# Kernel optimization log

Hardware: AMD Instinct MI355X
Metric: run time of the kernel (lower is better)

The kernel has to match this reference:

```python
import jax, jax.numpy as jnp
import numpy as np

CIN, HID, OUT = 128, 256, 349
NTYPES, ETYPES = 4, 5
N0, N1, N2 = 120000, 40000, 10000
GNODES, GEDGES = 250000, 2000000
E0, E1 = 1500000, 400000


def setup_inputs() -> dict:
    key = jax.random.key(0)
    ks = jax.random.split(key, 24)
    ri = jax.random.randint
    rn = jax.random.normal
    inp = {}
    inp['n_id'] = ri(ks[0], (N0,), 0, GNODES)
    inp['x0'] = rn(ks[1], (100000, CIN), dtype=jnp.float32)
    inp['src0'] = ri(ks[2], (E0,), 0, N0)
    inp['dst0'] = ri(ks[3], (E0,), 0, N1)
    inp['e_id0'] = ri(ks[4], (E0,), 0, GEDGES)
    inp['src1'] = ri(ks[5], (E1,), 0, N1)
    inp['dst1'] = ri(ks[6], (E1,), 0, N2)
    inp['e_id1'] = ri(ks[7], (E1,), 0, GEDGES)
    inp['edge_type'] = ri(ks[8], (GEDGES,), 0, ETYPES)
    inp['node_type'] = ri(ks[9], (GNODES,), 0, NTYPES)
    inp['local_node_idx'] = ri(ks[10], (GNODES,), 0, 50000)
    # learned parameters
    inp['emb1'] = rn(ks[11], (50000, CIN), dtype=jnp.float32)
    inp['emb2'] = rn(ks[12], (50000, CIN), dtype=jnp.float32)
    inp['emb3'] = rn(ks[13], (50000, CIN), dtype=jnp.float32)
    s0 = 1.0 / np.sqrt(CIN)
    s1 = 1.0 / np.sqrt(HID)
    inp['relW0'] = rn(ks[14], (ETYPES, CIN, HID), dtype=jnp.float32) * s0
    inp['rootW0'] = rn(ks[15], (NTYPES, CIN, HID), dtype=jnp.float32) * s0
    inp['rootb0'] = rn(ks[16], (NTYPES, HID), dtype=jnp.float32) * 0.02
    inp['relW1'] = rn(ks[17], (ETYPES, HID, OUT), dtype=jnp.float32) * s1
    inp['rootW1'] = rn(ks[18], (NTYPES, HID, OUT), dtype=jnp.float32) * s1
    inp['rootb1'] = rn(ks[19], (NTYPES, OUT), dtype=jnp.float32) * 0.02
    return inp


def _group_input(tables, node_type, local_node_idx, n_id):
    # RGNN.group_input: per-node-type gather from feature / embedding tables.
    nt = node_type[n_id]            # [N0]
    li = local_node_idx[n_id]       # [N0]
    h = jnp.zeros((n_id.shape[0], CIN), dtype=tables[0].dtype)
    for k, tab in enumerate(tables):
        idx = jnp.minimum(li, tab.shape[0] - 1)
        h = jnp.where((nt == k)[:, None], tab[idx], h)
    return h, nt


def _rgcn_layer(x, nt_src, src, dst, et, relW, rootW, rootb, n_tgt):
    # out = sum_t mean-aggregate(x_j over edges of type t) @ W_t  (linear commutes with mean)
    T = relW.shape[0]
    xj = x[src]                                           # [E, Cin] gather
    seg = dst * T + et                                    # fused (target, edge_type) segment id
    sums = jax.ops.segment_sum(xj, seg, num_segments=n_tgt * T)
    cnts = jax.ops.segment_sum(jnp.ones((src.shape[0],), x.dtype), seg, num_segments=n_tgt * T)
    mean = (sums / jnp.maximum(cnts, 1.0)[:, None]).reshape(n_tgt, T, -1)  # [Nt, T, Cin]
    out = jnp.einsum('ntc,tco->no', mean, relW)           # [Nt, Cout]
    # per-node-type root linear: out[mask] += root_lins[i](x_target[mask])
    x_t = x[:n_tgt]
    nt_t = nt_src[:n_tgt]
    allr = jnp.einsum('nc,tco->tno', x_t, rootW) + rootb[:, None, :]  # [Tn, Nt, Cout]
    root = jnp.take_along_axis(allr, nt_t[None, :, None], axis=0)[0]
    return out + root


def reference(n_id, x0, src0, dst0, e_id0, src1, dst1, e_id1, edge_type, node_type,
              local_node_idx, emb1, emb2, emb3, relW0, rootW0, rootb0, relW1, rootW1, rootb1):
    h, nt = _group_input([x0, emb1, emb2, emb3], node_type, local_node_idx, n_id)
    # layer 0: I -> H
    h = _rgcn_layer(h, nt, src0, dst0, edge_type[e_id0], relW0, rootW0, rootb0, N1)
    h = jax.nn.relu(h)
    nt = nt[:N1]
    # layer 1: H -> O
    h = _rgcn_layer(h, nt, src1, dst1, edge_type[e_id1], relW1, rootW1, rootb1, N2)
    return jax.nn.log_softmax(h, axis=-1)
```

## Files before the change

kernel.cpp:

```cpp
#include <hip/hip_runtime.h>
#include <hip/hip_bf16.h>
#include <cmath>

constexpr int kCIN = 128, kHID = 256, kOUT = 349;
constexpr int kNT = 4, kET = 5;
constexpr int kN0 = 120000, kN1 = 40000, kN2 = 10000;
constexpr int kNSEG0 = kN1 * kET;
constexpr int kNSEG1 = kN2 * kET;
constexpr int kNSEG = kNSEG0 + kNSEG1;

constexpr int kBinSegs = 512;
constexpr int kNBin0 = (kNSEG0 + kBinSegs - 1) / kBinSegs;
constexpr int kNBin1 = (kNSEG1 + kBinSegs - 1) / kBinSegs;
constexpr int kNBin  = kNBin0 + kNBin1;
constexpr int kNBLK  = 512;
constexpr int kSB    = 128;
constexpr int kGB    = (kN0 + 31) / 32;

typedef __bf16 bf16x8 __attribute__((ext_vector_type(8)));
typedef float f32x4 __attribute__((ext_vector_type(4)));
typedef float f32x2v __attribute__((ext_vector_type(2)));
typedef unsigned short ushort8v __attribute__((ext_vector_type(8)));

__device__ __forceinline__ unsigned short f2b(float f) {
    unsigned int b = __float_as_uint(f);
    unsigned int r = (b + 0x7FFFu + ((b >> 16) & 1u)) >> 16;
    return (unsigned short)r;
}
__device__ __forceinline__ float b2f(unsigned short u) {
    return __uint_as_float((unsigned int)u << 16);
}
__device__ __forceinline__ void gl2lds16(const void* g, void* l) {
    __builtin_amdgcn_global_load_lds(
        (const __attribute__((address_space(1))) void*)g,
        (__attribute__((address_space(3))) void*)l, 16, 0, 0);
}

__device__ __forceinline__ unsigned int f2e4m3(float f) {
#if __has_builtin(__builtin_amdgcn_cvt_pk_fp8_f32)
    return (unsigned int)(__builtin_amdgcn_cvt_pk_fp8_f32(f, f, 0, false) & 0xFF);
#else
    unsigned int sb = (__float_as_uint(f) >> 31) << 7;
    float m = fminf(fabsf(f), 448.f);
    unsigned int code;
    if (m < 0.015625f) {
        code = (unsigned int)__float2int_rn(m * 512.f);
    } else {
        unsigned int b = __float_as_uint(m);
        b = b + 0x7FFFF + ((b >> 20) & 1);
        int e8 = (int)(b >> 23) - 120;
        if (e8 > 15) code = 0x7E;
        else code = ((unsigned int)e8 << 3) | ((b >> 20) & 7);
    }
    return sb | code;
#endif
}

__device__ __forceinline__ void e4m3x4_to_f32(unsigned int u, float* o4) {
#if __has_builtin(__builtin_amdgcn_cvt_pk_f32_fp8)
    f32x2v a = __builtin_amdgcn_cvt_pk_f32_fp8(u, false);
    f32x2v b = __builtin_amdgcn_cvt_pk_f32_fp8(u, true);
    o4[0] = a[0]; o4[1] = a[1]; o4[2] = b[0]; o4[3] = b[1];
#else
#pragma unroll
    for (int i = 0; i < 4; i++) {
        unsigned int c = (u >> (8 * i)) & 0xFF;
        unsigned int s = c >> 7, e = (c >> 3) & 15, mm = c & 7;
        float v;
        if (e == 0) v = (float)mm * 0.001953125f;
        else        v = __uint_as_float((e + 120u) << 23 | mm << 20);
        o4[i] = s ? -v : v;
    }
#endif
}

__global__ void k_prep(const float* __restrict__ relW0, const float* __restrict__ rootW0,
                       unsigned short* __restrict__ Bt0T,
                       const float* __restrict__ relW1, const float* __restrict__ rootW1,
                       unsigned short* __restrict__ Bt1T,
                       const int* __restrict__ etype, unsigned char* __restrict__ et8, int nET)
{
    constexpr int T0 = kNT * 256 * 768;
    constexpr int T1 = kNT * 384 * 1536;
    constexpr int TP = T0 + T1;
    int i = blockIdx.x * 256 + threadIdx.x;
    if (i < T0) {
        int g = i / (256 * 768);
        int rem = i - g * (256 * 768);
        int col = rem / 768;
        int k = rem - col * 768;
        float v = (k < 640) ? relW0[(size_t)k * 256 + col]
                            : rootW0[((size_t)g * 128 + (k - 640)) * 256 + col];
        Bt0T[i] = f2b(v);
    } else if (i < TP) {
        int ii = i - T0;
        int g = ii / (384 * 1536);
        int rem = ii - g * (384 * 1536);
        int col = rem / 1536;
        int k = rem - col * 1536;
        float v = 0.f;
        if (col < kOUT) v = (k < 1280) ? relW1[(size_t)k * kOUT + col]
                                       : rootW1[((size_t)g * 256 + (k - 1280)) * kOUT + col];
        Bt1T[ii] = f2b(v);
    } else {
        int k = i - TP;
        if (k < nET) et8[k] = (unsigned char)etype[k];
    }
}

__global__ __launch_bounds__(1024) void k_bincnt(
    const int* __restrict__ dst0, const int* __restrict__ eid0, int E0,
    const int* __restrict__ dst1, const int* __restrict__ eid1, int E1,
    const unsigned char* __restrict__ et8, int* __restrict__ cnts2d,
    int* __restrict__ seg32,
    const int* __restrict__ n_id, const int* __restrict__ ntype, int* __restrict__ ntcnts,
    const float* __restrict__ x0, const float* __restrict__ e1f,
    const float* __restrict__ e2f, const float* __restrict__ e3f,
    const int* __restrict__ lidx,
    unsigned short* __restrict__ h0b, unsigned char* __restrict__ h0f8,
    int* __restrict__ nt0)
{
    __shared__ int h[kNBin];
    const int tid = threadIdx.x;
    if (blockIdx.x < kNBLK) {
        for (int k = tid; k < kNBin; k += 1024) h[k] = 0;
        __syncthreads();
        int Etot = E0 + E1;
        int chunk = (Etot + kNBLK - 1) / kNBLK;
        int lo = blockIdx.x * chunk;
        int hi = min(lo + chunk, Etot);
        for (int i = lo + tid; i < hi; i += 1024) {
            int c;
            if (i < E0) c = dst0[i] * kET + (int)et8[eid0[i]];
            else { int e = i - E0; c = kNBin0 * kBinSegs + dst1[e] * kET + (int)et8[eid1[e]]; }
            seg32[i] = c;
            atomicAdd(&h[c >> 9], 1);
        }
        __syncthreads();
        for (int k = tid; k < kNBin; k += 1024) cnts2d[(size_t)k * kNBLK + blockIdx.x] = h[k];
    } else if (blockIdx.x < kNBLK + 2 * kSB) {
        int b = blockIdx.x - kNBLK;
        int layer = b >= kSB;
        int blk = b - layer * kSB;
        int M = layer ? kN2 : kN1;
        if (tid < 4) h[tid] = 0;
        __syncthreads();
        int chunk = (M + kSB - 1) / kSB;
        int lo = blk * chunk, hi = min(lo + chunk, M);
        for (int i = lo + tid; i < hi; i += 1024) atomicAdd(&h[ntype[n_id[i]]], 1);
        __syncthreads();
        if (tid < 4) ntcnts[(layer * 4 + tid) * kSB + blk] = h[tid];
    } else {
        int row = (blockIdx.x - kNBLK - 2 * kSB) * 32 + (tid >> 5);
        if (row >= kN0) return;
        int lane = tid & 31;
        int gid = n_id[row];
        int nt = ntype[gid];
        int li = lidx[gid];
        const float* tab;
        int rows;
        if (nt == 0)      { tab = x0;  rows = 100000; }
        else if (nt == 1) { tab = e1f; rows = 50000; }
        else if (nt == 2) { tab = e2f; rows = 50000; }
        else              { tab = e3f; rows = 50000; }
        int idx = li < rows ? li : rows - 1;
        float4 v = reinterpret_cast<const float4*>(tab + (size_t)idx * kCIN)[lane];
        ushort4 o;
        o.x = f2b(v.x); o.y = f2b(v.y); o.z = f2b(v.z); o.w = f2b(v.w);
        reinterpret_cast<ushort4*>(h0b + (size_t)row * kCIN)[lane] = o;
        unsigned int q = f2e4m3(v.x) | (f2e4m3(v.y) << 8) | (f2e4m3(v.z) << 16) | (f2e4m3(v.w) << 24);
        reinterpret_cast<unsigned int*>(h0f8 + (size_t)row * kCIN)[lane] = q;
        if (lane == 0) nt0[row] = nt;
    }
}

__global__ void k_scan1(const int* __restrict__ cnt, int* __restrict__ excl,
                        int* __restrict__ blksum, int n)
{
    __shared__ int sm[1024];
    int i = blockIdx.x * 1024 + threadIdx.x;
    int v = (i < n) ? cnt[i] : 0;
    sm[threadIdx.x] = v;
    __syncthreads();
    for (int off = 1; off < 1024; off <<= 1) {
        int t = (threadIdx.x >= off) ? sm[threadIdx.x - off] : 0;
        __syncthreads();
        sm[threadIdx.x] += t;
        __syncthreads();
    }
    if (i < n) excl[i] = sm[threadIdx.x] - v;
    if (threadIdx.x == 1023) blksum[blockIdx.x] = sm[1023];
}

__global__ __launch_bounds__(1024) void k_scan2(
    int* __restrict__ blksum, int nblk,
    const int* __restrict__ ntcnts, int* __restrict__ ntoffs,
    int* __restrict__ goff0, int* __restrict__ goff1)
{
    __shared__ int sm[1024];
    int tid = threadIdx.x;
    if (blockIdx.x == 0) {
        int v = (tid < nblk) ? blksum[tid] : 0;
        sm[tid] = v;
        __syncthreads();
        for (int off = 1; off < 1024; off <<= 1) {
            int t = (tid >= off) ? sm[tid - off] : 0;
            __syncthreads();
            sm[tid] += t;
            __syncthreads();
        }
        if (tid < nblk) blksum[tid] = sm[tid] - v;
    } else {
        int v = ntcnts[tid];
        sm[tid] = v;
        __syncthreads();
        for (int off = 1; off < 512; off <<= 1) {
            int t = 0;
            if ((tid & 511) >= off) t = sm[tid - off];
            __syncthreads();
            sm[tid] += t;
            __syncthreads();
        }
        int excl = sm[tid] - v;
        ntoffs[tid] = excl;
        if ((tid & 127) == 0) {
            int layer = tid >> 9;
            int t = (tid >> 7) & 3;
            if (layer == 0) goff0[t] = excl; else goff1[t] = excl;
        }
        if (tid == 0) { goff0[4] = kN1; goff1[4] = kN2; }
    }
}

__global__ __launch_bounds__(1024) void k_binplace(
    const int* __restrict__ src0, int E0,
    const int* __restrict__ src1, int E1,
    const int* __restrict__ seg32,
    const int* __restrict__ offs2d, const int* __restrict__ blksum,
    unsigned int* __restrict__ pairs,
    const int* __restrict__ nt0, const int* __restrict__ ntoffs,
    int* __restrict__ perm0, int* __restrict__ perm1)
{
    __shared__ int cur[kNBin];
    const int tid = threadIdx.x;
    if (blockIdx.x < kNBLK) {
        for (int k = tid; k < kNBin; k += 1024) {
            size_t li = (size_t)k * kNBLK + blockIdx.x;
            cur[k] = offs2d[li] + blksum[li >> 10];
        }
        __syncthreads();
        int Etot = E0 + E1;
        int chunk = (Etot + kNBLK - 1) / kNBLK;
        int lo = blockIdx.x * chunk;
        int hi = min(lo + chunk, Etot);
        for (int i = lo + tid; i < hi; i += 1024) {
            int c = seg32[i];
            int s = (i < E0) ? src0[i] : src1[i - E0];
            unsigned int pay = (unsigned int)s | ((unsigned int)(c & (kBinSegs - 1)) << 17);
            int p = atomicAdd(&cur[c >> 9], 1);
            pairs[p] = pay;
        }
    } else {
        int b = blockIdx.x - kNBLK;
        int layer = b >= kSB;
        int blk = b - layer * kSB;
        int M = layer ? kN2 : kN1;
        int* perm = layer ? perm1 : perm0;
        if (tid < 4) cur[tid] = ntoffs[(layer * 4 + tid) * kSB + blk];
        __syncthreads();
        int chunk = (M + kSB - 1) / kSB;
        int lo = blk * chunk, hi = min(lo + chunk, M);
        for (int i = lo + tid; i < hi; i += 1024) {
            int p = atomicAdd(&cur[nt0[i]], 1);
            perm[p] = i;
        }
    }
}

__global__ __launch_bounds__(1024) void k_binscatter(
    const int* __restrict__ offs2d, const int* __restrict__ blksum, int Etot,
    const unsigned int* __restrict__ pairs,
    int* __restrict__ order, int* __restrict__ starts, int* __restrict__ cnt)
{
    __shared__ int h[kBinSegs];
    __shared__ int sc[kBinSegs];
    __shared__ int cur[kBinSegs];
    const int bin = blockIdx.x;
    const int tid = threadIdx.x;
    size_t bi = (size_t)bin * kNBLK;
    const int base = offs2d[bi] + blksum[bi >> 10];
    int end = Etot;
    if (bin + 1 < kNBin) {
        size_t ei = (size_t)(bin + 1) * kNBLK;
        end = offs2d[ei] + blksum[ei >> 10];
    }
    const int c = end - base;
    const unsigned int* pp = pairs + base;

    for (int k = tid; k < kBinSegs; k += 1024) h[k] = 0;
    __syncthreads();
    for (int j = tid; j < c; j += 1024) atomicAdd(&h[pp[j] >> 17], 1);
    __syncthreads();
    if (tid < kBinSegs) sc[tid] = h[tid];
    __syncthreads();
    for (int off = 1; off < kBinSegs; off <<= 1) {
        int t = 0;
        if (tid < kBinSegs && tid >= off) t = sc[tid - off];
        __syncthreads();
        if (tid < kBinSegs) sc[tid] += t;
        __syncthreads();
    }
    int seg_rel, abs_base, seglim;
    if (bin < kNBin0) { seg_rel = bin * kBinSegs; abs_base = seg_rel; seglim = kNSEG0 - seg_rel; }
    else { seg_rel = (bin - kNBin0) * kBinSegs; abs_base = kNSEG0 + seg_rel; seglim = kNSEG1 - seg_rel; }
    if (tid < kBinSegs) {
        int excl = sc[tid] - h[tid];
        cur[tid] = excl;
        if (tid < seglim) {
            starts[abs_base + tid] = base + excl;
            cnt[abs_base + tid] = h[tid];
        }
    }
    __syncthreads();
    for (int j = tid; j < c; j += 1024) {
        unsigned int u = pp[j];
        int sl = (int)(u >> 17);
        int p = atomicAdd(&cur[sl], 1);
        order[base + p] = (int)(u & 0x1FFFFu);
    }
}

template<int C>
__global__ __launch_bounds__(256) void k_segreduce8(
    const int* __restrict__ starts, const int* __restrict__ cnt,
    const int* __restrict__ order, const unsigned char* __restrict__ h8,
    unsigned short* __restrict__ mean, int nseg)
{
    constexpr int L = C / 16;
    constexpr int SPB = 256 / L;
    int sidx = blockIdx.x * SPB + threadIdx.x / L;
    if (sidx >= nseg) return;
    int lane = threadIdx.x % L;
    int st = starts[sidx];
    int n = cnt[sidx];
    const unsigned char* hp = h8 + (size_t)lane * 16;
    float a0[16], a1[16];
#pragma unroll
    for (int i = 0; i < 16; i++) { a0[i] = 0.f; a1[i] = 0.f; }
    int j = 0;
    for (; j + 2 <= n; j += 2) {
        int s0 = order[st + j + 0];
        int s1 = order[st + j + 1];
        uint4 u0 = *reinterpret_cast<const uint4*>(hp + (size_t)s0 * C);
        uint4 u1 = *reinterpret_cast<const uint4*>(hp + (size_t)s1 * C);
        float d[16];
        e4m3x4_to_f32(u0.x, d); e4m3x4_to_f32(u0.y, d + 4);
        e4m3x4_to_f32(u0.z, d + 8); e4m3x4_to_f32(u0.w, d + 12);
#pragma unroll
        for (int i = 0; i < 16; i++) a0[i] += d[i];
        e4m3x4_to_f32(u1.x, d); e4m3x4_to_f32(u1.y, d + 4);
        e4m3x4_to_f32(u1.z, d + 8); e4m3x4_to_f32(u1.w, d + 12);
#pragma unroll
        for (int i = 0; i < 16; i++) a1[i] += d[i];
    }
    if (j < n) {
        int s0 = order[st + j];
        uint4 u0 = *reinterpret_cast<const uint4*>(hp + (size_t)s0 * C);
        float d[16];
        e4m3x4_to_f32(u0.x, d); e4m3x4_to_f32(u0.y, d + 4);
        e4m3x4_to_f32(u0.z, d + 8); e4m3x4_to_f32(u0.w, d + 12);
#pragma unroll
        for (int i = 0; i < 16; i++) a0[i] += d[i];
    }
    float sc = 1.0f / fmaxf((float)n, 1.0f);
    ushort8v o0, o1;
#pragma unroll
    for (int i = 0; i < 8; i++) {
        o0[i] = f2b((a0[i] + a1[i]) * sc);
        o1[i] = f2b((a0[i + 8] + a1[i + 8]) * sc);
    }
    unsigned short* mp = mean + (size_t)sidx * C + lane * 16;
    *reinterpret_cast<ushort8v*>(mp) = o0;
    *reinterpret_cast<ushort8v*>(mp + 8) = o1;
}

template<int C, int BM, int BNF, int NCB, int WR, int WC, int RELU, int OUTBF16, int OUTF8>
__global__ __launch_bounds__(256) void k_gemm_sorted(
    int M, int Nreal, int NpadK,
    const unsigned short* __restrict__ meanb,
    const unsigned short* __restrict__ hb,
    const unsigned short* __restrict__ BtT,
    const float* __restrict__ rootb,
    const int* __restrict__ perm, const int* __restrict__ goff,
    unsigned short* __restrict__ outb, float* __restrict__ outf,
    unsigned char* __restrict__ outf8)
{
    constexpr int K1 = kET * C;
    constexpr int K  = K1 + C;
    constexpr int FM = BM / (16 * WR);
    constexpr int FN = BNF / (16 * WC);
    __shared__ __align__(16) char ldsA[BM * 128];
    __shared__ __align__(16) char ldsB[BNF * 128];

    int nwg = gridDim.x;
    int orig = blockIdx.x;
    int q = nwg >> 3, r8 = nwg & 7, x8 = orig & 7;
    int logical = (x8 < r8 ? x8 * (q + 1) : r8 * (q + 1) + (x8 - r8) * q) + (orig >> 3);
    int colb = logical % NCB;
    int t = logical / NCB;

    int g, row0s = 0, gend = 0;
    {
        int gs[5] = {goff[0], goff[1], goff[2], goff[3], goff[4]};
        int tb = 0;
        for (g = 0; g < 4; ++g) {
            int cg = gs[g + 1] - gs[g];
            int ntl = (cg + BM - 1) / BM;
            if (t < tb + ntl) { row0s = gs[g] + (t - tb) * BM; gend = gs[g + 1]; break; }
            tb += ntl;
        }
        if (g == 4) return;
    }
    const int rows_here = min(BM, gend - row0s);
    const unsigned short* BtG = BtT + (size_t)g * NpadK;

    const int tid = threadIdx.x;
    const int col0 = colb * BNF;
    const int wid = tid >> 6, lane = tid & 63;
    const int wrow = (wid / WC) * (BM / WR);
    const int wcol = (wid % WC) * (BNF / WC);
    const int lr = lane >> 3;
    const int kb = (lane & 7) * 16;

    f32x4 acc[FM][FN] = {};

    for (int k0 = 0; k0 < K; k0 += 64) {
        const bool inMean = (k0 < K1);
        const size_t kB = (size_t)k0 * 2;
#pragma unroll
        for (int c2 = 0; c2 < BM / 32; ++c2) {
            int rb = (wid * (BM / 32) + c2) * 8;
            int r = rb + lr;
            int pr = perm[row0s + min(r, rows_here - 1)];
            const char* rowp = inMean
                ? (const char*)(meanb + (size_t)pr * K1) + kB
                : (const char*)(hb + (size_t)pr * C) + (kB - (size_t)K1 * 2);
            gl2lds16(rowp + (kb ^ ((r & 7) << 4)), &ldsA[rb * 128]);
        }
#pragma unroll
        for (int c2 = 0; c2 < BNF / 32; ++c2) {
            int rb = (wid * (BNF / 32) + c2) * 8;
            int r = rb + lr;
            const char* rowp = (const char*)(BtG + (size_t)(col0 + r) * K) + kB;
            gl2lds16(rowp + (kb ^ ((r & 7) << 4)), &ldsB[rb * 128]);
        }
        __syncthreads();
#pragma unroll
        for (int kc = 0; kc < 2; kc++) {
            int kb2 = kc * 64 + (lane >> 4) * 16;
            bf16x8 af[FM], bfr[FN];
#pragma unroll
            for (int m = 0; m < FM; m++) {
                int r = wrow + m * 16 + (lane & 15);
                af[m] = *reinterpret_cast<const bf16x8*>(&ldsA[r * 128 + (kb2 ^ ((r & 7) << 4))]);
            }
#pragma unroll
            for (int n = 0; n < FN; n++) {
                int r = wcol + n * 16 + (lane & 15);
                bfr[n] = *reinterpret_cast<const bf16x8*>(&ldsB[r * 128 + (kb2 ^ ((r & 7) << 4))]);
            }
#pragma unroll
            for (int m = 0; m < FM; m++)
#pragma unroll
                for (int n = 0; n < FN; n++)
                    acc[m][n] = __builtin_amdgcn_mfma_f32_16x16x32_bf16(af[m], bfr[n], acc[m][n], 0, 0, 0);
        }
        __syncthreads();
    }

#pragma unroll
    for (int m = 0; m < FM; m++) {
        int rlb = wrow + m * 16 + (lane >> 4) * 4;
#pragma unroll
        for (int n = 0; n < FN; n++) {
            int col = col0 + wcol + n * 16 + (lane & 15);
            if (col >= Nreal) continue;
            f32x4 v = acc[m][n];
#pragma unroll
            for (int j = 0; j < 4; j++) {
                int rl = rlb + j;
                if (rl >= rows_here) continue;
                int orig_row = perm[row0s + rl];
                float xv = v[j] + rootb[g * Nreal + col];
                if (RELU) xv = fmaxf(xv, 0.f);
                if (OUTBF16) {
                    outb[(size_t)orig_row * Nreal + col] = f2b(xv);
                    if (OUTF8) outf8[(size_t)orig_row * Nreal + col] = (unsigned char)f2e4m3(xv);
                } else {
                    outf[(size_t)orig_row * Nreal + col] = xv;
                }
            }
        }
    }
}

__global__ void k_logsm(float* __restrict__ out, int M, int N)
{
    int row = blockIdx.x * 4 + (threadIdx.x >> 6);
    if (row >= M) return;
    int lane = threadIdx.x & 63;
    float* p = out + (size_t)row * N;
    float mx = -3.4e38f;
    for (int c = lane; c < N; c += 64) mx = fmaxf(mx, p[c]);
#pragma unroll
    for (int o = 32; o > 0; o >>= 1) mx = fmaxf(mx, __shfl_xor(mx, o));
    float s = 0.f;
    for (int c = lane; c < N; c += 64) s += expf(p[c] - mx);
#pragma unroll
    for (int o = 32; o > 0; o >>= 1) s += __shfl_xor(s, o);
    float lse = mx + logf(s);
    for (int c = lane; c < N; c += 64) p[c] -= lse;
}

extern "C" void kernel_launch(void* const* d_in, const int* in_sizes, int n_in,
                              void* d_out, int out_size, void* d_ws, size_t ws_size,
                              hipStream_t stream)
{
    const int*   n_id   = (const int*)d_in[0];
    const float* x0     = (const float*)d_in[1];
    const int*   src0   = (const int*)d_in[2];
    const int*   dst0   = (const int*)d_in[3];
    const int*   eid0   = (const int*)d_in[4];
    const int*   src1   = (const int*)d_in[5];
    const int*   dst1   = (const int*)d_in[6];
    const int*   eid1   = (const int*)d_in[7];
    const int*   etype  = (const int*)d_in[8];
    const int*   ntype  = (const int*)d_in[9];
    const int*   lidx   = (const int*)d_in[10];
    const float* emb1   = (const float*)d_in[11];
    const float* emb2   = (const float*)d_in[12];
    const float* emb3   = (const float*)d_in[13];
    const float* relW0  = (const float*)d_in[14];
    const float* rootW0 = (const float*)d_in[15];
    const float* rootb0 = (const float*)d_in[16];
    const float* relW1  = (const float*)d_in[17];
    const float* rootW1 = (const float*)d_in[18];
    const float* rootb1 = (const float*)d_in[19];
    float* out = (float*)d_out;

    const int E0 = in_sizes[2];
    const int E1 = in_sizes[5];
    const int Etot = E0 + E1;
    const int nET = in_sizes[8];
    constexpr int K0s  = kET * kCIN + kCIN;
    constexpr int K1s  = kET * kHID + kHID;
    constexpr int Npad0 = 256;
    constexpr int Npad1 = 384;

    char* ws = (char*)d_ws;
    size_t off = 0;
    auto alloc = [&](size_t bytes) -> void* {
        void* p = ws + off;
        off = (off + bytes + 255) & ~(size_t)255;
        return p;
    };
    unsigned short* h0b   = (unsigned short*)alloc((size_t)kN0 * kCIN * 2);
    unsigned char*  h0f8  = (unsigned char*)alloc((size_t)kN0 * kCIN);
    int*            nt0   = (int*)alloc((size_t)kN0 * 4);
    unsigned short* meanb = (unsigned short*)alloc((size_t)kNSEG0 * kCIN * 2);
    int*            cnt    = (int*)alloc((size_t)kNSEG * 4);
    int*            starts = (int*)alloc((size_t)kNSEG * 4);
    int*            cnts2d = (int*)alloc((size_t)kNBin * kNBLK * 4);
    int*            offs2d = (int*)alloc((size_t)kNBin * kNBLK * 4);
    int*            blksum = (int*)alloc(1024 * 4);
    unsigned int*   pairs  = (unsigned int*)alloc((size_t)Etot * 4);
    int*            order  = (int*)alloc((size_t)Etot * 4);
    int*            seg32  = (int*)alloc((size_t)Etot * 4);
    unsigned char*  et8    = (unsigned char*)alloc((size_t)nET);
    unsigned short* h1b   = (unsigned short*)alloc((size_t)kN1 * kHID * 2);
    unsigned char*  h1f8  = (unsigned char*)alloc((size_t)kN1 * kHID);
    unsigned short* Bt0T  = (unsigned short*)alloc((size_t)kNT * Npad0 * K0s * 2);
    unsigned short* Bt1T  = (unsigned short*)alloc((size_t)kNT * Npad1 * K1s * 2);
    int*            perm0  = (int*)alloc((size_t)kN1 * 4);
    int*            goff0  = (int*)alloc(8 * 4);
    int*            perm1  = (int*)alloc((size_t)kN2 * 4);
    int*            goff1  = (int*)alloc(8 * 4);
    int*            ntcnts = (int*)alloc(1024 * 4);
    int*            ntoffs = (int*)alloc(1024 * 4);

    constexpr int TPREP = kNT * Npad0 * K0s + kNT * Npad1 * K1s;
    int prep_total = TPREP + nET;
    k_prep<<<(prep_total + 255) / 256, 256, 0, stream>>>(relW0, rootW0, Bt0T, relW1, rootW1, Bt1T,
                                                         etype, et8, nET);

    k_bincnt<<<kNBLK + 2 * kSB + kGB, 1024, 0, stream>>>(
        dst0, eid0, E0, dst1, eid1, E1, et8, cnts2d, seg32,
        n_id, ntype, ntcnts, x0, emb1, emb2, emb3, lidx, h0b, h0f8, nt0);

    int nscan = kNBin * kNBLK;
    int nblk = (nscan + 1023) / 1024;
    k_scan1<<<nblk, 1024, 0, stream>>>(cnts2d, offs2d, blksum, nscan);
    k_scan2<<<2, 1024, 0, stream>>>(blksum, nblk, ntcnts, ntoffs, goff0, goff1);
    k_binplace<<<kNBLK + 2 * kSB, 1024, 0, stream>>>(src0, E0, src1, E1, seg32,
                                                     offs2d, blksum, pairs, nt0, ntoffs, perm0, perm1);
    k_binscatter<<<kNBin, 1024, 0, stream>>>(offs2d, blksum, Etot, pairs, order, starts, cnt);

    k_segreduce8<kCIN><<<(kNSEG0 + 31) / 32, 256, 0, stream>>>(starts, cnt, order, h0f8, meanb, kNSEG0);
    int g0 = (kN1 / 64 + 4) * 2;
    k_gemm_sorted<kCIN, 64, 128, 2, 2, 2, 1, 1, 1><<<g0, 256, 0, stream>>>(
        kN1, kHID, Npad0 * K0s, meanb, h0b, Bt0T, rootb0, perm0, goff0, h1b, nullptr, h1f8);

    k_segreduce8<kHID><<<(kNSEG1 + 15) / 16, 256, 0, stream>>>(starts + kNSEG0, cnt + kNSEG0, order, h1f8, meanb, kNSEG1);
    int g1 = (kN2 / 64 + 5) * 3;
    k_gemm_sorted<kHID, 64, 128, 3, 2, 2, 0, 0, 0><<<g1, 256, 0, stream>>>(
        kN2, kOUT, Npad1 * K1s, meanb, h1b, Bt1T, rootb1, perm1, goff1, nullptr, out, nullptr);

    k_logsm<<<(kN2 + 3) / 4, 256, 0, stream>>>(out, kN2, kOUT);
}
```

Measured before the change: 236.3 us.

## Drop bf16 hidden copy, feed layer-1 root GEMM from fp8; two rows per gather warp

Layer 0 now writes only the fp8 hidden activations, dropping the separate bf16 copy. Layer 1's root-term A tiles are decoded from fp8 to bf16 in registers and stored to LDS, replacing the async global-to-LDS load. The input gather now handles two rows per half-warp to raise memory-level parallelism, and the binning block count is halved. This removes about 20 MB of writes but lowers root-term precision to fp8 and adds decode work inside the GEMM K-loop.

```diff
diff --git a/kernel.cpp b/kernel.cpp
--- a/kernel.cpp
+++ b/kernel.cpp
@@ -13,9 +13,9 @@
 constexpr int kNBin0 = (kNSEG0 + kBinSegs - 1) / kBinSegs;
 constexpr int kNBin1 = (kNSEG1 + kBinSegs - 1) / kBinSegs;
 constexpr int kNBin  = kNBin0 + kNBin1;
-constexpr int kNBLK  = 512;
+constexpr int kNBLK  = 256;
 constexpr int kSB    = 128;
-constexpr int kGB    = (kN0 + 31) / 32;
+constexpr int kGB    = kN0 / 64;
 
 typedef __bf16 bf16x8 __attribute__((ext_vector_type(8)));
 typedef float f32x4 __attribute__((ext_vector_type(4)));
@@ -151,26 +151,37 @@
         __syncthreads();
         if (tid < 4) ntcnts[(layer * 4 + tid) * kSB + blk] = h[tid];
     } else {
-        int row = (blockIdx.x - kNBLK - 2 * kSB) * 32 + (tid >> 5);
-        if (row >= kN0) return;
+        int base = (blockIdx.x - kNBLK - 2 * kSB) * 64;
         int lane = tid & 31;
-        int gid = n_id[row];
-        int nt = ntype[gid];
-        int li = lidx[gid];
-        const float* tab;
-        int rows;
-        if (nt == 0)      { tab = x0;  rows = 100000; }
-        else if (nt == 1) { tab = e1f; rows = 50000; }
-        else if (nt == 2) { tab = e2f; rows = 50000; }
-        else              { tab = e3f; rows = 50000; }
-        int idx = li < rows ? li : rows - 1;
-        float4 v = reinterpret_cast<const float4*>(tab + (size_t)idx * kCIN)[lane];
-        ushort4 o;
-        o.x = f2b(v.x); o.y = f2b(v.y); o.z = f2b(v.z); o.w = f2b(v.w);
-        reinterpret_cast<ushort4*>(h0b + (size_t)row * kCIN)[lane] = o;
-        unsigned int q = f2e4m3(v.x) | (f2e4m3(v.y) << 8) | (f2e4m3(v.z) << 16) | (f2e4m3(v.w) << 24);
-        reinterpret_cast<unsigned int*>(h0f8 + (size_t)row * kCIN)[lane] = q;
-        if (lane == 0) nt0[row] = nt;
+        int r0 = base + (tid >> 5);
+        int r1 = r0 + 32;
+        int gid0 = n_id[r0], gid1 = n_id[r1];
+        int nta = ntype[gid0], ntb = ntype[gid1];
+        int lia = lidx[gid0], lib = lidx[gid1];
+        const float* taba; int rowsa;
+        if (nta == 0)      { taba = x0;  rowsa = 100000; }
+        else if (nta == 1) { taba = e1f; rowsa = 50000; }
+        else if (nta == 2) { taba = e2f; rowsa = 50000; }
+        else               { taba = e3f; rowsa = 50000; }
+        const float* tabb; int rowsb;
+        if (ntb == 0)      { tabb = x0;  rowsb = 100000; }
+        else if (ntb == 1) { tabb = e1f; rowsb = 50000; }
+        else if (ntb == 2) { tabb = e2f; rowsb = 50000; }
+        else               { tabb = e3f; rowsb = 50000; }
+        int ia = lia < rowsa ? lia : rowsa - 1;
+        int ib = lib < rowsb ? lib : rowsb - 1;
+        float4 v0 = reinterpret_cast<const float4*>(taba + (size_t)ia * kCIN)[lane];
+        float4 v1 = reinterpret_cast<const float4*>(tabb + (size_t)ib * kCIN)[lane];
+        ushort4 o0, o1;
+        o0.x = f2b(v0.x); o0.y = f2b(v0.y); o0.z = f2b(v0.z); o0.w = f2b(v0.w);
+        o1.x = f2b(v1.x); o1.y = f2b(v1.y); o1.z = f2b(v1.z); o1.w = f2b(v1.w);
+        reinterpret_cast<ushort4*>(h0b + (size_t)r0 * kCIN)[lane] = o0;
+        reinterpret_cast<ushort4*>(h0b + (size_t)r1 * kCIN)[lane] = o1;
+        unsigned int q0 = f2e4m3(v0.x) | (f2e4m3(v0.y) << 8) | (f2e4m3(v0.z) << 16) | (f2e4m3(v0.w) << 24);
+        unsigned int q1 = f2e4m3(v1.x) | (f2e4m3(v1.y) << 8) | (f2e4m3(v1.z) << 16) | (f2e4m3(v1.w) << 24);
+        reinterpret_cast<unsigned int*>(h0f8 + (size_t)r0 * kCIN)[lane] = q0;
+        reinterpret_cast<unsigned int*>(h0f8 + (size_t)r1 * kCIN)[lane] = q1;
+        if (lane == 0) { nt0[r0] = nta; nt0[r1] = ntb; }
     }
 }
 
@@ -384,16 +395,16 @@
     *reinterpret_cast<ushort8v*>(mp + 8) = o1;
 }
 
-template<int C, int BM, int BNF, int NCB, int WR, int WC, int RELU, int OUTBF16, int OUTF8>
+template<int C, int BM, int BNF, int NCB, int WR, int WC, int RELU, int AF8, int OUTF32>
 __global__ __launch_bounds__(256) void k_gemm_sorted(
     int M, int Nreal, int NpadK,
     const unsigned short* __restrict__ meanb,
     const unsigned short* __restrict__ hb,
+    const unsigned char* __restrict__ hb8,
     const unsigned short* __restrict__ BtT,
     const float* __restrict__ rootb,
     const int* __restrict__ perm, const int* __restrict__ goff,
-    unsigned short* __restrict__ outb, float* __restrict__ outf,
-    unsigned char* __restrict__ outf8)
+    float* __restrict__ outf, unsigned char* __restrict__ outf8)
 {
     constexpr int K1 = kET * C;
     constexpr int K  = K1 + C;
@@ -437,15 +448,32 @@
     for (int k0 = 0; k0 < K; k0 += 64) {
         const bool inMean = (k0 < K1);
         const size_t kB = (size_t)k0 * 2;
-#pragma unroll
-        for (int c2 = 0; c2 < BM / 32; ++c2) {
-            int rb = (wid * (BM / 32) + c2) * 8;
-            int r = rb + lr;
-            int pr = perm[row0s + min(r, rows_here - 1)];
-            const char* rowp = inMean
-                ? (const char*)(meanb + (size_t)pr * K1) + kB
-                : (const char*)(hb + (size_t)pr * C) + (kB - (size_t)K1 * 2);
-            gl2lds16(rowp + (kb ^ ((r & 7) << 4)), &ldsA[rb * 128]);
+        if (!AF8 || inMean) {
+#pragma unroll
+            for (int c2 = 0; c2 < BM / 32; ++c2) {
+                int rb = (wid * (BM / 32) + c2) * 8;
+                int r = rb + lr;
+                int pr = perm[row0s + min(r, rows_here - 1)];
+                const char* rowp = inMean
+                    ? (const char*)(meanb + (size_t)pr * K1) + kB
+                    : (const char*)(hb + (size_t)pr * C) + (kB - (size_t)K1 * 2);
+                gl2lds16(rowp + (kb ^ ((r & 7) << 4)), &ldsA[rb * 128]);
+            }
+        } else {
+#pragma unroll
+            for (int c2 = 0; c2 < BM / 32; ++c2) {
+                int rb = (wid * (BM / 32) + c2) * 8;
+                int r = rb + lr;
+                int pr = perm[row0s + min(r, rows_here - 1)];
+                int eo = (k0 - K1) + ((kb ^ ((r & 7) << 4)) >> 1);
+                uint2 u = *reinterpret_cast<const uint2*>(hb8 + (size_t)pr * C + eo);
+                float d[8];
+                e4m3x4_to_f32(u.x, d); e4m3x4_to_f32(u.y, d + 4);
+                ushort8v o;
+#pragma unroll
+                for (int i = 0; i < 8; i++) o[i] = f2b(d[i]);
+                *reinterpret_cast<ushort8v*>(&ldsA[rb * 128 + lane * 16]) = o;
+            }
         }
 #pragma unroll
         for (int c2 = 0; c2 < BNF / 32; ++c2) {
@@ -493,12 +521,8 @@
                 int orig_row = perm[row0s + rl];
                 float xv = v[j] + rootb[g * Nreal + col];
                 if (RELU) xv = fmaxf(xv, 0.f);
-                if (OUTBF16) {
-                    outb[(size_t)orig_row * Nreal + col] = f2b(xv);
-                    if (OUTF8) outf8[(size_t)orig_row * Nreal + col] = (unsigned char)f2e4m3(xv);
-                } else {
-                    outf[(size_t)orig_row * Nreal + col] = xv;
-                }
+                if (OUTF32) outf[(size_t)orig_row * Nreal + col] = xv;
+                else        outf8[(size_t)orig_row * Nreal + col] = (unsigned char)f2e4m3(xv);
             }
         }
     }
@@ -577,7 +601,6 @@
     int*            order  = (int*)alloc((size_t)Etot * 4);
     int*            seg32  = (int*)alloc((size_t)Etot * 4);
     unsigned char*  et8    = (unsigned char*)alloc((size_t)nET);
-    unsigned short* h1b   = (unsigned short*)alloc((size_t)kN1 * kHID * 2);
     unsigned char*  h1f8  = (unsigned char*)alloc((size_t)kN1 * kHID);
     unsigned short* Bt0T  = (unsigned short*)alloc((size_t)kNT * Npad0 * K0s * 2);
     unsigned short* Bt1T  = (unsigned short*)alloc((size_t)kNT * Npad1 * K1s * 2);
@@ -607,13 +630,13 @@
 
     k_segreduce8<kCIN><<<(kNSEG0 + 31) / 32, 256, 0, stream>>>(starts, cnt, order, h0f8, meanb, kNSEG0);
     int g0 = (kN1 / 64 + 4) * 2;
-    k_gemm_sorted<kCIN, 64, 128, 2, 2, 2, 1, 1, 1><<<g0, 256, 0, stream>>>(
-        kN1, kHID, Npad0 * K0s, meanb, h0b, Bt0T, rootb0, perm0, goff0, h1b, nullptr, h1f8);
+    k_gemm_sorted<kCIN, 64, 128, 2, 2, 2, 1, 0, 0><<<g0, 256, 0, stream>>>(
+        kN1, kHID, Npad0 * K0s, meanb, h0b, nullptr, Bt0T, rootb0, perm0, goff0, nullptr, h1f8);
 
     k_segreduce8<kHID><<<(kNSEG1 + 15) / 16, 256, 0, stream>>>(starts + kNSEG0, cnt + kNSEG0, order, h1f8, meanb, kNSEG1);
     int g1 = (kN2 / 64 + 5) * 3;
-    k_gemm_sorted<kHID, 64, 128, 3, 2, 2, 0, 0, 0><<<g1, 256, 0, stream>>>(
-        kN2, kOUT, Npad1 * K1s, meanb, h1b, Bt1T, rootb1, perm1, goff1, nullptr, out, nullptr);
+    k_gemm_sorted<kHID, 64, 128, 3, 2, 2, 0, 1, 1><<<g1, 256, 0, stream>>>(
+        kN2, kOUT, Npad1 * K1s, meanb, nullptr, h1f8, Bt1T, rootb1, perm1, goff1, out, nullptr);
 
     k_logsm<<<(kN2 + 3) / 4, 256, 0, stream>>>(out, kN2, kOUT);
 }
```

Result: faster. 219.8 us (-7.0%).
